# Kernel optimization log

Hardware: AMD Instinct MI355X
Metric: run time of the kernel (lower is better)

## Reference

```python
import jax, jax.numpy as jnp
import numpy as np
from jax import lax


def conv2d(x, w, b=None, stride=1, pad=0, groups=1):
    # x: [N,C,H,W], w: [Cout, Cin/groups, kh, kw]
    out = lax.conv_general_dilated(
        x, w, window_strides=(stride, stride),
        padding=[(pad, pad), (pad, pad)],
        feature_group_count=groups,
        dimension_numbers=('NCHW', 'OIHW', 'NCHW'))
    if b is not None:
        out = out + b[None, :, None, None]
    return out


def deform_conv2d(x, offsets, weight, stride=1, pad=1, dil=1, groups=1):
    # x: [N,C,H,W]; offsets: [N, 2*K, Ho, Wo] with (dy,dx) interleaved per kernel tap
    # weight: [Cout, C/groups, kh, kw]
    N, C, H, W = x.shape
    Cout, Cg, kh, kw = weight.shape
    K = kh * kw
    Ho = (H + 2 * pad - dil * (kh - 1) - 1) // stride + 1
    Wo = (W + 2 * pad - dil * (kw - 1) - 1) // stride + 1

    off = offsets.reshape(N, K, 2, Ho, Wo)
    # base sampling grid: p0 + kernel tap offset
    base_h = (jnp.arange(Ho) * stride - pad).astype(x.dtype)  # [Ho]
    base_w = (jnp.arange(Wo) * stride - pad).astype(x.dtype)  # [Wo]
    ki = jnp.repeat(jnp.arange(kh), kw).astype(x.dtype) * dil  # [K]
    kj = jnp.tile(jnp.arange(kw), kh).astype(x.dtype) * dil    # [K]
    py = base_h[None, None, :, None] + ki[None, :, None, None] + off[:, :, 0]  # [N,K,Ho,Wo]
    px = base_w[None, None, None, :] + kj[None, :, None, None] + off[:, :, 1]  # [N,K,Ho,Wo]

    y0 = jnp.floor(py); x0 = jnp.floor(px)
    wy = py - y0; wx = px - x0  # bilinear weights, [N,K,Ho,Wo]
    y0i = y0.astype(jnp.int32); x0i = x0.astype(jnp.int32)

    xf = x.reshape(N, C, H * W)

    def gather(yi, xi):
        valid = (yi >= 0) & (yi < H) & (xi >= 0) & (xi < W)
        yc = jnp.clip(yi, 0, H - 1)
        xc = jnp.clip(xi, 0, W - 1)
        idx = (yc * W + xc).reshape(N, 1, K * Ho * Wo)
        g = jnp.take_along_axis(xf, idx, axis=2).reshape(N, C, K, Ho, Wo)
        return g * valid.astype(x.dtype)[:, None]  # zero padding outside

    v00 = gather(y0i, x0i)
    v01 = gather(y0i, x0i + 1)
    v10 = gather(y0i + 1, x0i)
    v11 = gather(y0i + 1, x0i + 1)
    wy_ = wy[:, None]; wx_ = wx[:, None]  # [N,1,K,Ho,Wo]
    sampled = (v00 * (1 - wy_) * (1 - wx_) + v01 * (1 - wy_) * wx_
               + v10 * wy_ * (1 - wx_) + v11 * wy_ * wx_)  # [N,C,K,Ho,Wo]

    g = groups
    sampled = sampled.reshape(N, g, Cg, K, Ho, Wo)
    wg = weight.reshape(g, Cout // g, Cg, K)
    out = jnp.einsum('ngckhw,gock->ngohw', sampled, wg)
    return out.reshape(N, Cout, Ho, Wo)


def setup_inputs() -> dict:
    key = jax.random.key(0)
    ks = jax.random.split(key, 6)
    N, C, H, W = 8, 256, 64, 64
    offc = 18  # 2*3*3
    return {
        'x': jax.random.normal(ks[0], (N, C, H, W), jnp.float32),
        'w_adj': jax.random.normal(ks[1], (offc, C, 1, 1), jnp.float32) * 0.05,
        'b_adj': jax.random.normal(ks[2], (offc,), jnp.float32) * 0.05,
        'w_off': jax.random.normal(ks[3], (offc, 1, 3, 3), jnp.float32) * 0.05,
        'b_off': jax.random.normal(ks[4], (offc,), jnp.float32) * 0.05,
        'w_def': jax.random.normal(ks[5], (C, C, 3, 3), jnp.float32) * 0.02,
    }


def reference(x, w_adj, b_adj, w_off, b_off, w_def):
    x_chan = conv2d(x, w_adj, b_adj, stride=1, pad=0)            # 1x1 conv -> 18 ch
    offsets = conv2d(x_chan, w_off, b_off, stride=1, pad=1, groups=18)  # depthwise 3x3
    out = deform_conv2d(x, offsets, w_def, stride=1, pad=1, dil=1, groups=1)
    return out
```

## Files before the change

kernel.cpp:

```cpp
#include <hip/hip_runtime.h>


typedef __attribute__((ext_vector_type(8))) short short8v;
typedef __attribute__((ext_vector_type(4))) float f32x4;

#define NPLANE 4096

__device__ inline unsigned bf16_1(float a) {
    unsigned u = __float_as_uint(a);
    u += 0x7fffu + ((u >> 16) & 1u);
    return u >> 16;
}
__device__ inline unsigned bf16_pair(float a, float b) {
    unsigned ua = __float_as_uint(a); ua += 0x7fffu + ((ua >> 16) & 1u);
    unsigned ub = __float_as_uint(b); ub += 0x7fffu + ((ub >> 16) & 1u);
    return (ua >> 16) | (ub & 0xffff0000u);
}
__device__ inline unsigned cvt_pk(float lo, float hi) {
    unsigned r;
    asm("v_cvt_pk_bf16_f32 %0, %1, %2" : "=v"(r) : "v"(lo), "v"(hi));
    return r;
}
__device__ inline float bl(unsigned u) { return __uint_as_float(u << 16); }
__device__ inline float bh(unsigned u) { return __uint_as_float(u & 0xffff0000u); }

__device__ inline void block_sync_lgkm() {
    asm volatile("s_waitcnt lgkmcnt(0)" ::: "memory");
    __builtin_amdgcn_s_barrier();
    __builtin_amdgcn_sched_barrier(0);
}

__global__ __launch_bounds__(256) void k_prep(const float* __restrict__ x,
                                              const float* __restrict__ w_adj,
                                              const float* __restrict__ b_adj,
                                              const float* __restrict__ w_def,
                                              float* __restrict__ xchan,
                                              ushort* __restrict__ wfrag,
                                              ushort* __restrict__ xT) {
    __shared__ float wsh[256][18];
    __shared__ float part[8][32][19];
    __shared__ unsigned tileU[64][35];
    int b = blockIdx.x;
    int t = threadIdx.x;
    if (b < 1024) {
        for (int i = t; i < 18 * 256; i += 256) {
            int o = i >> 8, c = i & 255;
            wsh[c][o] = w_adj[i];
        }
        __syncthreads();
        int n    = b >> 7;
        int pix0 = (b & 127) << 5;
        int p = t & 31, g = t >> 5;
        const float* xp = x + ((size_t)n << 20) + ((size_t)g << 17) + pix0 + p;
        float acc[18];
#pragma unroll
        for (int o = 0; o < 18; ++o) acc[o] = 0.f;
#pragma unroll 4
        for (int ci = 0; ci < 32; ++ci) {
            float xv = xp[(size_t)ci << 12];
            const float* wr = wsh[(g << 5) + ci];
#pragma unroll
            for (int o = 0; o < 18; ++o) acc[o] = fmaf(xv, wr[o], acc[o]);
        }
#pragma unroll
        for (int o = 0; o < 18; ++o) part[g][p][o] = acc[o];
        __syncthreads();
        for (int i = t; i < 576; i += 256) {
            int o = i >> 5, p2 = i & 31;
            float s = b_adj[o];
#pragma unroll
            for (int g2 = 0; g2 < 8; ++g2) s += part[g2][p2][o];
            xchan[((size_t)n * 18 + o) * NPLANE + pix0 + p2] = s;
        }
    } else if (b < 3328) {
        int idx = (b - 1024) * 256 + t;
        int e     = idx & 7;
        int lane  = (idx >> 3) & 63;
        int ct    = (idx >> 9) & 15;
        int kstep = idx >> 13;
        int cout = ct * 16 + (lane & 15);
        int c    = ((kstep & 7) << 5) + ((lane >> 4) << 3) + e;
        int tap  = kstep >> 3;
        float v = w_def[cout * 2304 + c * 9 + tap];
        wfrag[idx] = (ushort)bf16_1(v);
    } else {
        int bb = b - 3328;
        int n  = bb & 7;
        int cg = (bb >> 3) & 3;
        int pg = bb >> 5;
        int pl = t & 63, c4 = t >> 6;
        const float* src = x + (((size_t)(n * 256 + cg * 64 + c4 * 16)) << 12)
                             + (pg << 6) + pl;
#pragma unroll
        for (int i2 = 0; i2 < 8; ++i2) {
            float f0 = src[(size_t)(2 * i2) << 12];
            float f1 = src[(size_t)(2 * i2 + 1) << 12];
            tileU[pl][c4 * 8 + i2] = bf16_pair(f0, f1);
        }
        __syncthreads();
        int cl2 = t & 31, pr = t >> 5;
        unsigned* dst = (unsigned*)xT;
#pragma unroll
        for (int i = 0; i < 8; ++i) {
            int p2 = pr + (i << 3);
            dst[((size_t)(n << 12) + (pg << 6) + p2) * 128 + (cg << 5) + cl2] =
                tileU[p2][cl2];
        }
    }
}

__global__ __launch_bounds__(256) void k_off(const float* __restrict__ xchan,
                                             const float* __restrict__ w_off,
                                             const float* __restrict__ b_off,
                                             float* __restrict__ off) {
    int idx = blockIdx.x * 256 + threadIdx.x;
    int pix = idx & 4095;
    int w = pix & 63, h = pix >> 6;
    int rest = idx >> 12;
    int oc = rest % 18;
    const float* wp  = w_off + oc * 9;
    const float* src = xchan + (idx & ~4095);
    float acc = b_off[oc];
#pragma unroll
    for (int i = 0; i < 3; ++i) {
        int hh = h - 1 + i;
        if ((unsigned)hh >= 64u) continue;
#pragma unroll
        for (int j = 0; j < 3; ++j) {
            int ww = w - 1 + j;
            if ((unsigned)ww >= 64u) continue;
            acc = fmaf(src[(hh << 6) + ww], wp[i * 3 + j], acc);
        }
    }
    off[idx] = acc;
}

__global__ __launch_bounds__(256) void k_fused(const ushort* __restrict__ xT,
                                               const float* __restrict__ off,
                                               const ushort* __restrict__ wfrag,
                                               float* __restrict__ out) {
    __shared__ __align__(16) ushort colS[2][2][2][64][8];

    int t = threadIdx.x;
    int wv = t >> 6, lane = t & 63;
    int n  = blockIdx.x & 7;
    int tq = blockIdx.x >> 3;

    int ksp  = t >> 7;
    int tile = (t >> 6) & 1;
    int pix  = (t >> 2) & 15;
    int cg   = t & 3;
    int sc   = cg << 3;
    int spix = (tq << 5) + (tile << 4) + pix;
    int sy = spix >> 6, sx = spix & 63;

    const float* offn = off + (((size_t)n * 18) << 12) + spix;
    const ushort* xTn = xT + (((size_t)n) << 12) * 256;

    int wslot = (cg << 4) | ((pix ^ (cg << 1)) & 15);
    ushort* wp0 = &colS[0][ksp][tile][wslot][0];
    ushort* wp1 = &colS[1][ksp][tile][wslot][0];

    float w00, w01, w10, w11;
    unsigned oA, oB, oC, oD;

    auto tap_setup = [&](int tp) {
        float oyv = offn[(size_t)(2 * tp) << 12];
        float oxv = offn[(size_t)(2 * tp + 1) << 12];
        int trow = (tp * 11) >> 5;
        int tcol = tp - trow * 3;
        float py = (float)(sy - 1 + trow) + oyv;
        float px = (float)(sx - 1 + tcol) + oxv;
        float fy = floorf(py), fx = floorf(px);
        int y0 = (int)fy, x0 = (int)fx;
        float wy1 = py - fy, wx1 = px - fx;
        float ay0 = ((unsigned)y0       < 64u) ? 1.f - wy1 : 0.f;
        float ay1 = ((unsigned)(y0 + 1) < 64u) ? wy1 : 0.f;
        float ax0 = ((unsigned)x0       < 64u) ? 1.f - wx1 : 0.f;
        float ax1 = ((unsigned)(x0 + 1) < 64u) ? wx1 : 0.f;
        w00 = ay0 * ax0; w01 = ay0 * ax1; w10 = ay1 * ax0; w11 = ay1 * ax1;
        int yc0 = min(max(y0, 0), 63), yc1 = min(max(y0 + 1, 0), 63);
        int xc0 = min(max(x0, 0), 63), xc1 = min(max(x0 + 1, 0), 63);
        oA = (unsigned)((((yc0 << 6) + xc0) << 8) + sc);
        oB = (unsigned)((((yc0 << 6) + xc1) << 8) + sc);
        oC = (unsigned)((((yc1 << 6) + xc0) << 8) + sc);
        oD = (unsigned)((((yc1 << 6) + xc1) << 8) + sc);
    };

    uint4 gA, gB, gC, gD;
    auto issue = [&](int m) {
        unsigned dd = (unsigned)(((2 * m + ksp) & 7) << 5);
        gA = *(const uint4*)(xTn + oA + dd);
        gB = *(const uint4*)(xTn + oB + dd);
        gC = *(const uint4*)(xTn + oC + dd);
        gD = *(const uint4*)(xTn + oD + dd);
    };
    auto interp_to = [&](ushort* wp) {
        unsigned qa[4] = {gA.x, gA.y, gA.z, gA.w};
        unsigned qb[4] = {gB.x, gB.y, gB.z, gB.w};
        unsigned qc[4] = {gC.x, gC.y, gC.z, gC.w};
        unsigned qd[4] = {gD.x, gD.y, gD.z, gD.w};
        unsigned rr[4];
#pragma unroll
        for (int i = 0; i < 4; ++i) {
            float v0 = w00 * bl(qa[i]) + w01 * bl(qb[i]) +
                       w10 * bl(qc[i]) + w11 * bl(qd[i]);
            float v1 = w00 * bh(qa[i]) + w01 * bh(qb[i]) +
                       w10 * bh(qc[i]) + w11 * bh(qd[i]);
            rr[i] = cvt_pk(v0, v1);
        }
        *(uint4*)wp = make_uint4(rr[0], rr[1], rr[2], rr[3]);
    };

    f32x4 acc[2][4] = {};
    const int ctb = wv << 2;

    short8v bbA[4], bbB[4], bbN[4];
    auto loadW = [&](int ks, short8v* dst) {
        const ushort* wb = wfrag + ((size_t)ks * 16 + ctb) * 512 + (lane << 3);
#pragma unroll
        for (int j = 0; j < 4; ++j)
            dst[j] = *(const short8v*)(wb + (size_t)j * 512);
    };

    const int rslot = ((lane >> 4) << 4) | ((lane & 15) ^ ((lane >> 4) << 1));

    tap_setup(0);
    issue(0);
    interp_to(wp0);
    issue(1);
    loadW(0, bbA);
    block_sync_lgkm();

    for (int bt2 = 0; bt2 < 18; ++bt2) {
#pragma unroll
        for (int ph = 0; ph < 2; ++ph) {
            const int bt = bt2 * 2 + ph;
            const ushort* rb = &colS[ph][0][0][0][0];
            short8v a00 = *(const short8v*)(rb + ((0 * 64 + rslot) << 3));
            short8v a01 = *(const short8v*)(rb + ((1 * 64 + rslot) << 3));
            short8v a10 = *(const short8v*)(rb + ((2 * 64 + rslot) << 3));
            short8v a11 = *(const short8v*)(rb + ((3 * 64 + rslot) << 3));
            loadW(2 * bt + 1, bbB);
            if (bt + 1 < 36) loadW(2 * bt + 2, bbN);
            if (bt + 1 < 36) interp_to(ph ? wp0 : wp1);
            if (bt + 2 < 36) {
                if (((bt + 2) & 3) == 0) tap_setup((bt + 2) >> 2);
                issue(bt + 2);
            }
#pragma unroll
            for (int j = 0; j < 4; ++j) {
                acc[0][j] = __builtin_amdgcn_mfma_f32_16x16x32_bf16(
                    bbA[j], a00, acc[0][j], 0, 0, 0);
                acc[1][j] = __builtin_amdgcn_mfma_f32_16x16x32_bf16(
                    bbA[j], a01, acc[1][j], 0, 0, 0);
            }
#pragma unroll
            for (int j = 0; j < 4; ++j) {
                acc[0][j] = __builtin_amdgcn_mfma_f32_16x16x32_bf16(
                    bbB[j], a10, acc[0][j], 0, 0, 0);
                acc[1][j] = __builtin_amdgcn_mfma_f32_16x16x32_bf16(
                    bbB[j], a11, acc[1][j], 0, 0, 0);
            }
            block_sync_lgkm();
#pragma unroll
            for (int j = 0; j < 4; ++j) bbA[j] = bbN[j];
        }
    }

    int cl = lane & 15;
    int ch = (lane >> 4) << 2;
    float* outn = out + ((size_t)n << 20);
#pragma unroll
    for (int i = 0; i < 2; ++i) {
        int opix = (tq << 5) + (i << 4) + cl;
#pragma unroll
        for (int j = 0; j < 4; ++j) {
            int cout = ((ctb + j) << 4) + ch;
            float* op = outn + ((size_t)cout << 12) + opix;
#pragma unroll
            for (int rr = 0; rr < 4; ++rr) op[(size_t)rr << 12] = acc[i][j][rr];
        }
    }
}

__global__ __launch_bounds__(256) void k_xchan(const float* __restrict__ x,
                                               const float* __restrict__ w_adj,
                                               const float* __restrict__ b_adj,
                                               float* __restrict__ xchan) {
    __shared__ float wsh[256][18];
    __shared__ float part[8][32][19];
    int t = threadIdx.x;
    for (int i = t; i < 18 * 256; i += 256) {
        int o = i >> 8, c = i & 255;
        wsh[c][o] = w_adj[i];
    }
    __syncthreads();
    int n    = blockIdx.x >> 7;
    int pix0 = (blockIdx.x & 127) << 5;
    int p = t & 31, g = t >> 5;
    const float* xp = x + ((size_t)n << 20) + ((size_t)g << 17) + pix0 + p;
    float acc[18];
#pragma unroll
    for (int o = 0; o < 18; ++o) acc[o] = 0.f;
#pragma unroll 4
    for (int ci = 0; ci < 32; ++ci) {
        float xv = xp[(size_t)ci << 12];
        const float* wr = wsh[(g << 5) + ci];
#pragma unroll
        for (int o = 0; o < 18; ++o) acc[o] = fmaf(xv, wr[o], acc[o]);
    }
#pragma unroll
    for (int o = 0; o < 18; ++o) part[g][p][o] = acc[o];
    __syncthreads();
    for (int i = t; i < 576; i += 256) {
        int o = i >> 5, p2 = i & 31;
        float s = b_adj[o];
#pragma unroll
        for (int g2 = 0; g2 < 8; ++g2) s += part[g2][p2][o];
        xchan[((size_t)n * 18 + o) * NPLANE + pix0 + p2] = s;
    }
}

__global__ __launch_bounds__(256) void k_reorder(const float* __restrict__ w_def,
                                                 float* __restrict__ w_t) {
    int idx = blockIdx.x * 256 + threadIdx.x;
    int co = idx & 255;
    int c  = (idx >> 8) & 255;
    int k  = idx >> 16;
    w_t[idx] = w_def[co * 2304 + c * 9 + k];
}

__global__ __launch_bounds__(256) void k_deform(const float* __restrict__ x,
                                                const float* __restrict__ off,
                                                const float* __restrict__ w_t,
                                                float* __restrict__ out) {
    __shared__ float colS[16][64];
    __shared__ float wS[16][128];
    __shared__ int   sy0[64], sx0[64];
    __shared__ float swy[64], swx[64];
    int t   = threadIdx.x;
    int n   = blockIdx.x >> 6;
    int h   = blockIdx.x & 63;
    int co0 = blockIdx.y << 7;
    float acc[4][8];
#pragma unroll
    for (int i = 0; i < 4; ++i)
#pragma unroll
        for (int j = 0; j < 8; ++j) acc[i][j] = 0.f;
    int tp = t & 15, tc = t >> 4;
    int cc_b = t >> 4, p0_b = (t & 15) << 2;
    const float* xn = x + (n << 20);
    for (int k = 0; k < 9; ++k) {
        if (t < 64) {
            const float* offp = off + ((n * 18 + 2 * k) << 12) + (h << 6);
            float oyv = offp[t];
            float oxv = offp[4096 + t];
            float py = (float)(h - 1 + k / 3) + oyv;
            float px = (float)(t - 1 + k % 3) + oxv;
            float fy = floorf(py), fx = floorf(px);
            sy0[t] = (int)fy; sx0[t] = (int)fx;
            swy[t] = py - fy; swx[t] = px - fx;
        }
        for (int c0 = 0; c0 < 256; c0 += 16) {
            __syncthreads();
            const float* base = xn + ((c0 + cc_b) << 12);
#pragma unroll
            for (int u = 0; u < 4; ++u) {
                int p = p0_b + u;
                int y0 = sy0[p], x0 = sx0[p];
                float wy = swy[p], wx = swx[p];
                float v00 = 0.f, v01 = 0.f, v10 = 0.f, v11 = 0.f;
                bool oky0 = (unsigned)y0 < 64u, oky1 = (unsigned)(y0 + 1) < 64u;
                bool okx0 = (unsigned)x0 < 64u, okx1 = (unsigned)(x0 + 1) < 64u;
                int r0 = (y0 << 6) + x0;
                if (oky0 && okx0) v00 = base[r0];
                if (oky0 && okx1) v01 = base[r0 + 1];
                if (oky1 && okx0) v10 = base[r0 + 64];
                if (oky1 && okx1) v11 = base[r0 + 65];
                colS[cc_b][p] = (v00 * (1.f - wx) + v01 * wx) * (1.f - wy) +
                                (v10 * (1.f - wx) + v11 * wx) * wy;
            }
            const float* wt = w_t + (k << 16) + (c0 << 8) + co0;
#pragma unroll
            for (int i = 0; i < 2; ++i) {
                int fi = i * 256 + t;
                int cc = fi >> 5;
                int cf = (fi & 31) << 2;
                *(float4*)&wS[cc][cf] = *(const float4*)&wt[(cc << 8) + cf];
            }
            __syncthreads();
#pragma unroll
            for (int kk = 0; kk < 16; ++kk) {
                float4 cv = *(const float4*)&colS[kk][tp << 2];
                float4 w0 = *(const float4*)&wS[kk][tc << 3];
                float4 w1 = *(const float4*)&wS[kk][(tc << 3) + 4];
                float cva[4] = {cv.x, cv.y, cv.z, cv.w};
                float wa[8]  = {w0.x, w0.y, w0.z, w0.w, w1.x, w1.y, w1.z, w1.w};
#pragma unroll
                for (int i = 0; i < 4; ++i)
#pragma unroll
                    for (int j = 0; j < 8; ++j)
                        acc[i][j] = fmaf(cva[i], wa[j], acc[i][j]);
            }
        }
    }
    int ob = (n << 20) + ((co0 + (tc << 3)) << 12) + (h << 6) + (tp << 2);
#pragma unroll
    for (int j = 0; j < 8; ++j) {
        float4 v = {acc[0][j], acc[1][j], acc[2][j], acc[3][j]};
        *(float4*)&out[ob + (j << 12)] = v;
    }
}

extern "C" void kernel_launch(void* const* d_in, const int* in_sizes, int n_in,
                              void* d_out, int out_size, void* d_ws, size_t ws_size,
                              hipStream_t stream) {
    const float* x     = (const float*)d_in[0];
    const float* w_adj = (const float*)d_in[1];
    const float* b_adj = (const float*)d_in[2];
    const float* w_off = (const float*)d_in[3];
    const float* b_off = (const float*)d_in[4];
    const float* w_def = (const float*)d_in[5];
    float* out = (float*)d_out;

    char* ws = (char*)d_ws;
    float* xchan = (float*)ws;
    float* off   = (float*)(ws + 2359296);

    const size_t NEED = 22675456;
    if (ws_size >= NEED) {
        ushort* wfrag = (ushort*)(ws + 4718592);
        ushort* xT    = (ushort*)(ws + 5898240);
        k_prep<<<5376, 256, 0, stream>>>(x, w_adj, b_adj, w_def,
                                         xchan, wfrag, xT);
        k_off<<<2304, 256, 0, stream>>>(xchan, w_off, b_off, off);
        k_fused<<<1024, 256, 0, stream>>>(xT, off, wfrag, out);
    } else {
        float* w_t = (float*)(ws + 4718592);
        k_xchan<<<1024, 256, 0, stream>>>(x, w_adj, b_adj, xchan);
        k_off<<<2304, 256, 0, stream>>>(xchan, w_off, b_off, off);
        k_reorder<<<2304, 256, 0, stream>>>(w_def, w_t);
        k_deform<<<dim3(512, 2), 256, 0, stream>>>(x, off, w_t, out);
    }
}
```

Baseline: 94.93 us.

## Double pixel tile per block in fused deform conv to reuse weights

Each block of the fused deform-conv GEMM kernel now covers 64 output pixels instead of 32, with all 256 threads sampling distinct pixels rather than splitting the K dimension across two thread halves. Every weight fragment loaded into registers now feeds four MFMA pixel tiles instead of two, so weight traffic per output is halved and the grid shrinks to 512 blocks. The cost is twice as many accumulator registers, twice as many barrier-separated K steps per block, and fewer blocks to spread across the CUs.

```diff
diff --git a/kernel.cpp b/kernel.cpp
--- a/kernel.cpp
+++ b/kernel.cpp
@@ -139,27 +139,26 @@
                                                const float* __restrict__ off,
                                                const ushort* __restrict__ wfrag,
                                                float* __restrict__ out) {
-    __shared__ __align__(16) ushort colS[2][2][2][64][8];
+    __shared__ __align__(16) ushort colS[2][4][64][8];
 
     int t = threadIdx.x;
     int wv = t >> 6, lane = t & 63;
     int n  = blockIdx.x & 7;
     int tq = blockIdx.x >> 3;
 
-    int ksp  = t >> 7;
-    int tile = (t >> 6) & 1;
-    int pix  = (t >> 2) & 15;
-    int cg   = t & 3;
-    int sc   = cg << 3;
-    int spix = (tq << 5) + (tile << 4) + pix;
+    int p6 = t >> 2;
+    int cg = t & 3;
+    int sc = cg << 3;
+    int spix = (tq << 6) + p6;
     int sy = spix >> 6, sx = spix & 63;
 
     const float* offn = off + (((size_t)n * 18) << 12) + spix;
     const ushort* xTn = xT + (((size_t)n) << 12) * 256;
 
-    int wslot = (cg << 4) | ((pix ^ (cg << 1)) & 15);
-    ushort* wp0 = &colS[0][ksp][tile][wslot][0];
-    ushort* wp1 = &colS[1][ksp][tile][wslot][0];
+    int wtile = p6 >> 4;
+    int wslot = (cg << 4) | (((p6 & 15) ^ (cg << 1)) & 15);
+    ushort* wp0 = &colS[0][wtile][wslot][0];
+    ushort* wp1 = &colS[1][wtile][wslot][0];
 
     float w00, w01, w10, w11;
     unsigned oA, oB, oC, oD;
@@ -188,8 +187,8 @@
     };
 
     uint4 gA, gB, gC, gD;
-    auto issue = [&](int m) {
-        unsigned dd = (unsigned)(((2 * m + ksp) & 7) << 5);
+    auto issue = [&](int k) {
+        unsigned dd = (unsigned)((k & 7) << 5);
         gA = *(const uint4*)(xTn + oA + dd);
         gB = *(const uint4*)(xTn + oB + dd);
         gC = *(const uint4*)(xTn + oC + dd);
@@ -212,10 +211,10 @@
         *(uint4*)wp = make_uint4(rr[0], rr[1], rr[2], rr[3]);
     };
 
-    f32x4 acc[2][4] = {};
+    f32x4 acc[4][4] = {};
     const int ctb = wv << 2;
 
-    short8v bbA[4], bbB[4], bbN[4];
+    short8v bbE[4], bbO[4];
     auto loadW = [&](int ks, short8v* dst) {
         const ushort* wb = wfrag + ((size_t)ks * 16 + ctb) * 512 + (lane << 3);
 #pragma unroll
@@ -229,42 +228,37 @@
     issue(0);
     interp_to(wp0);
     issue(1);
-    loadW(0, bbA);
+    loadW(0, bbE);
     block_sync_lgkm();
 
-    for (int bt2 = 0; bt2 < 18; ++bt2) {
+    for (int it = 0; it < 36; ++it) {
 #pragma unroll
         for (int ph = 0; ph < 2; ++ph) {
-            const int bt = bt2 * 2 + ph;
-            const ushort* rb = &colS[ph][0][0][0][0];
-            short8v a00 = *(const short8v*)(rb + ((0 * 64 + rslot) << 3));
-            short8v a01 = *(const short8v*)(rb + ((1 * 64 + rslot) << 3));
-            short8v a10 = *(const short8v*)(rb + ((2 * 64 + rslot) << 3));
-            short8v a11 = *(const short8v*)(rb + ((3 * 64 + rslot) << 3));
-            loadW(2 * bt + 1, bbB);
-            if (bt + 1 < 36) loadW(2 * bt + 2, bbN);
-            if (bt + 1 < 36) interp_to(ph ? wp0 : wp1);
-            if (bt + 2 < 36) {
-                if (((bt + 2) & 3) == 0) tap_setup((bt + 2) >> 2);
-                issue(bt + 2);
+            const int k = it * 2 + ph;
+            const ushort* rb = &colS[ph][0][0][0];
+            short8v a0 = *(const short8v*)(rb + ((0 * 64 + rslot) << 3));
+            short8v a1 = *(const short8v*)(rb + ((1 * 64 + rslot) << 3));
+            short8v a2 = *(const short8v*)(rb + ((2 * 64 + rslot) << 3));
+            short8v a3 = *(const short8v*)(rb + ((3 * 64 + rslot) << 3));
+            if (k + 1 < 72) loadW(k + 1, ph ? bbE : bbO);
+            if (k + 1 < 72) interp_to(ph ? wp0 : wp1);
+            if (k + 2 < 72) {
+                if (((k + 2) & 7) == 0) tap_setup((k + 2) >> 3);
+                issue(k + 2);
             }
+            const short8v* bb = ph ? bbO : bbE;
 #pragma unroll
             for (int j = 0; j < 4; ++j) {
                 acc[0][j] = __builtin_amdgcn_mfma_f32_16x16x32_bf16(
-                    bbA[j], a00, acc[0][j], 0, 0, 0);
+                    bb[j], a0, acc[0][j], 0, 0, 0);
                 acc[1][j] = __builtin_amdgcn_mfma_f32_16x16x32_bf16(
-                    bbA[j], a01, acc[1][j], 0, 0, 0);
-            }
-#pragma unroll
-            for (int j = 0; j < 4; ++j) {
-                acc[0][j] = __builtin_amdgcn_mfma_f32_16x16x32_bf16(
-                    bbB[j], a10, acc[0][j], 0, 0, 0);
-                acc[1][j] = __builtin_amdgcn_mfma_f32_16x16x32_bf16(
-                    bbB[j], a11, acc[1][j], 0, 0, 0);
+                    bb[j], a1, acc[1][j], 0, 0, 0);
+                acc[2][j] = __builtin_amdgcn_mfma_f32_16x16x32_bf16(
+                    bb[j], a2, acc[2][j], 0, 0, 0);
+                acc[3][j] = __builtin_amdgcn_mfma_f32_16x16x32_bf16(
+                    bb[j], a3, acc[3][j], 0, 0, 0);
             }
             block_sync_lgkm();
-#pragma unroll
-            for (int j = 0; j < 4; ++j) bbA[j] = bbN[j];
         }
     }
 
@@ -272,8 +266,8 @@
     int ch = (lane >> 4) << 2;
     float* outn = out + ((size_t)n << 20);
 #pragma unroll
-    for (int i = 0; i < 2; ++i) {
-        int opix = (tq << 5) + (i << 4) + cl;
+    for (int i = 0; i < 4; ++i) {
+        int opix = (tq << 6) + (i << 4) + cl;
 #pragma unroll
         for (int j = 0; j < 4; ++j) {
             int cout = ((ctb + j) << 4) + ch;
@@ -435,7 +429,7 @@
         k_prep<<<5376, 256, 0, stream>>>(x, w_adj, b_adj, w_def,
                                          xchan, wfrag, xT);
         k_off<<<2304, 256, 0, stream>>>(xchan, w_off, b_off, off);
-        k_fused<<<1024, 256, 0, stream>>>(xT, off, wfrag, out);
+        k_fused<<<512, 256, 0, stream>>>(xT, off, wfrag, out);
     } else {
         float* w_t = (float*)(ws + 4718592);
         k_xchan<<<1024, 256, 0, stream>>>(x, w_adj, b_adj, xchan);
```

Result: faster. 84.82 us (-10.7%).

## Enlarge fused deform tile to 64 pixels with 512-thread blocks

Applied to the files above, without the earlier changes.

The fused deformable-conv kernel now processes 64 output pixels per block with 8 waves instead of 32 pixels with 4 waves. Each wave covers 2 output-channel tiles across 4 pixel tiles rather than 4 across 2. This halves the weight fragment loads per wave per step and halves the grid, so each weight fetch feeds more MFMAs. In exchange each block has more threads at the barrier, uses twice the LDS for the sampled columns, and has fewer blocks to spread across CUs.

```diff
diff --git a/kernel.cpp b/kernel.cpp
--- a/kernel.cpp
+++ b/kernel.cpp
@@ -135,31 +135,32 @@
     off[idx] = acc;
 }
 
-__global__ __launch_bounds__(256) void k_fused(const ushort* __restrict__ xT,
+__global__ __launch_bounds__(512) void k_fused(const ushort* __restrict__ xT,
                                                const float* __restrict__ off,
                                                const ushort* __restrict__ wfrag,
                                                float* __restrict__ out) {
-    __shared__ __align__(16) ushort colS[2][2][2][64][8];
+    __shared__ __align__(16) ushort colS[2][2][4][64][8];
 
     int t = threadIdx.x;
     int wv = t >> 6, lane = t & 63;
     int n  = blockIdx.x & 7;
     int tq = blockIdx.x >> 3;
 
-    int ksp  = t >> 7;
-    int tile = (t >> 6) & 1;
-    int pix  = (t >> 2) & 15;
-    int cg   = t & 3;
-    int sc   = cg << 3;
-    int spix = (tq << 5) + (tile << 4) + pix;
+    int ksp = t >> 8;
+    int r_  = t & 255;
+    int p6  = r_ >> 2;
+    int cg  = r_ & 3;
+    int sc  = cg << 3;
+    int spix = (tq << 6) + p6;
     int sy = spix >> 6, sx = spix & 63;
 
     const float* offn = off + (((size_t)n * 18) << 12) + spix;
     const ushort* xTn = xT + (((size_t)n) << 12) * 256;
 
-    int wslot = (cg << 4) | ((pix ^ (cg << 1)) & 15);
-    ushort* wp0 = &colS[0][ksp][tile][wslot][0];
-    ushort* wp1 = &colS[1][ksp][tile][wslot][0];
+    int wtile = p6 >> 4;
+    int wslot = (cg << 4) | (((p6 & 15) ^ (cg << 1)) & 15);
+    ushort* wp0 = &colS[0][ksp][wtile][wslot][0];
+    ushort* wp1 = &colS[1][ksp][wtile][wslot][0];
 
     float w00, w01, w10, w11;
     unsigned oA, oB, oC, oD;
@@ -212,14 +213,14 @@
         *(uint4*)wp = make_uint4(rr[0], rr[1], rr[2], rr[3]);
     };
 
-    f32x4 acc[2][4] = {};
-    const int ctb = wv << 2;
-
-    short8v bbA[4], bbB[4], bbN[4];
+    f32x4 acc[4][2] = {};
+    const int ctb = wv << 1;
+
+    short8v bbA[2], bbB[2], bbN[2];
     auto loadW = [&](int ks, short8v* dst) {
         const ushort* wb = wfrag + ((size_t)ks * 16 + ctb) * 512 + (lane << 3);
 #pragma unroll
-        for (int j = 0; j < 4; ++j)
+        for (int j = 0; j < 2; ++j)
             dst[j] = *(const short8v*)(wb + (size_t)j * 512);
     };
 
@@ -237,10 +238,10 @@
         for (int ph = 0; ph < 2; ++ph) {
             const int bt = bt2 * 2 + ph;
             const ushort* rb = &colS[ph][0][0][0][0];
-            short8v a00 = *(const short8v*)(rb + ((0 * 64 + rslot) << 3));
-            short8v a01 = *(const short8v*)(rb + ((1 * 64 + rslot) << 3));
-            short8v a10 = *(const short8v*)(rb + ((2 * 64 + rslot) << 3));
-            short8v a11 = *(const short8v*)(rb + ((3 * 64 + rslot) << 3));
+            short8v ae0 = *(const short8v*)(rb + ((0 * 64 + rslot) << 3));
+            short8v ae1 = *(const short8v*)(rb + ((1 * 64 + rslot) << 3));
+            short8v ae2 = *(const short8v*)(rb + ((2 * 64 + rslot) << 3));
+            short8v ae3 = *(const short8v*)(rb + ((3 * 64 + rslot) << 3));
             loadW(2 * bt + 1, bbB);
             if (bt + 1 < 36) loadW(2 * bt + 2, bbN);
             if (bt + 1 < 36) interp_to(ph ? wp0 : wp1);
@@ -249,22 +250,34 @@
                 issue(bt + 2);
             }
 #pragma unroll
-            for (int j = 0; j < 4; ++j) {
+            for (int j = 0; j < 2; ++j) {
                 acc[0][j] = __builtin_amdgcn_mfma_f32_16x16x32_bf16(
-                    bbA[j], a00, acc[0][j], 0, 0, 0);
+                    bbA[j], ae0, acc[0][j], 0, 0, 0);
                 acc[1][j] = __builtin_amdgcn_mfma_f32_16x16x32_bf16(
-                    bbA[j], a01, acc[1][j], 0, 0, 0);
-            }
-#pragma unroll
-            for (int j = 0; j < 4; ++j) {
+                    bbA[j], ae1, acc[1][j], 0, 0, 0);
+                acc[2][j] = __builtin_amdgcn_mfma_f32_16x16x32_bf16(
+                    bbA[j], ae2, acc[2][j], 0, 0, 0);
+                acc[3][j] = __builtin_amdgcn_mfma_f32_16x16x32_bf16(
+                    bbA[j], ae3, acc[3][j], 0, 0, 0);
+            }
+            short8v ao0 = *(const short8v*)(rb + (((4 + 0) * 64 + rslot) << 3));
+            short8v ao1 = *(const short8v*)(rb + (((4 + 1) * 64 + rslot) << 3));
+            short8v ao2 = *(const short8v*)(rb + (((4 + 2) * 64 + rslot) << 3));
+            short8v ao3 = *(const short8v*)(rb + (((4 + 3) * 64 + rslot) << 3));
+#pragma unroll
+            for (int j = 0; j < 2; ++j) {
                 acc[0][j] = __builtin_amdgcn_mfma_f32_16x16x32_bf16(
-                    bbB[j], a10, acc[0][j], 0, 0, 0);
+                    bbB[j], ao0, acc[0][j], 0, 0, 0);
                 acc[1][j] = __builtin_amdgcn_mfma_f32_16x16x32_bf16(
-                    bbB[j], a11, acc[1][j], 0, 0, 0);
+                    bbB[j], ao1, acc[1][j], 0, 0, 0);
+                acc[2][j] = __builtin_amdgcn_mfma_f32_16x16x32_bf16(
+                    bbB[j], ao2, acc[2][j], 0, 0, 0);
+                acc[3][j] = __builtin_amdgcn_mfma_f32_16x16x32_bf16(
+                    bbB[j], ao3, acc[3][j], 0, 0, 0);
             }
             block_sync_lgkm();
 #pragma unroll
-            for (int j = 0; j < 4; ++j) bbA[j] = bbN[j];
+            for (int j = 0; j < 2; ++j) bbA[j] = bbN[j];
         }
     }
 
@@ -272,10 +285,10 @@
     int ch = (lane >> 4) << 2;
     float* outn = out + ((size_t)n << 20);
 #pragma unroll
-    for (int i = 0; i < 2; ++i) {
-        int opix = (tq << 5) + (i << 4) + cl;
-#pragma unroll
-        for (int j = 0; j < 4; ++j) {
+    for (int i = 0; i < 4; ++i) {
+        int opix = (tq << 6) + (i << 4) + cl;
+#pragma unroll
+        for (int j = 0; j < 2; ++j) {
             int cout = ((ctb + j) << 4) + ch;
             float* op = outn + ((size_t)cout << 12) + opix;
 #pragma unroll
@@ -435,7 +448,7 @@
         k_prep<<<5376, 256, 0, stream>>>(x, w_adj, b_adj, w_def,
                                          xchan, wfrag, xT);
         k_off<<<2304, 256, 0, stream>>>(xchan, w_off, b_off, off);
-        k_fused<<<1024, 256, 0, stream>>>(xT, off, wfrag, out);
+        k_fused<<<512, 512, 0, stream>>>(xT, off, wfrag, out);
     } else {
         float* w_t = (float*)(ws + 4718592);
         k_xchan<<<1024, 256, 0, stream>>>(x, w_adj, b_adj, xchan);
```

Measured after the change: 83.85 us. 11.7% less time.

## Fuse 1x1 conv with bf16 transpose and enlarge deform GEMM tile to 1024 threads

Applied to the files above, without the earlier changes.

In the prep kernel, the 1x1 offset-channel convolution and the bf16 pixel-major transpose of x now run in the same blocks, so x is read once from global memory instead of twice. The fused deform kernel moves from 256-thread blocks covering 32 pixels to 1024-thread blocks covering 128 pixels, with 16 waves arranged as 4 pixel groups by 4 output-channel groups. Each weight fragment loaded from global memory is therefore reused across more pixels, and the B-fragment double buffering is simplified. The cost is more LDS per block, only 256 blocks for the whole grid, and block-wide barriers across 16 waves, which may hurt occupancy and latency hiding.

```diff
diff --git a/kernel.cpp b/kernel.cpp
--- a/kernel.cpp
+++ b/kernel.cpp
@@ -37,43 +37,56 @@
                                               float* __restrict__ xchan,
                                               ushort* __restrict__ wfrag,
                                               ushort* __restrict__ xT) {
-    __shared__ float wsh[256][18];
-    __shared__ float part[8][32][19];
-    __shared__ unsigned tileU[64][35];
+    __shared__ unsigned tileU[64][133];
+    __shared__ float    ubuf[5120];
     int b = blockIdx.x;
     int t = threadIdx.x;
-    if (b < 1024) {
-        for (int i = t; i < 18 * 256; i += 256) {
+    if (b < 512) {
+        int n  = b & 7;
+        int pg = b >> 3;
+        int pl = t & 63, c4 = t >> 6;
+        for (int i = t; i < 4608; i += 256) {
             int o = i >> 8, c = i & 255;
-            wsh[c][o] = w_adj[i];
+            ubuf[c * 20 + o] = w_adj[i];
         }
         __syncthreads();
-        int n    = b >> 7;
-        int pix0 = (b & 127) << 5;
-        int p = t & 31, g = t >> 5;
-        const float* xp = x + ((size_t)n << 20) + ((size_t)g << 17) + pix0 + p;
-        float acc[18];
-#pragma unroll
-        for (int o = 0; o < 18; ++o) acc[o] = 0.f;
+        const float* xp = x + (((size_t)(n * 256 + c4 * 64)) << 12)
+                            + (pg << 6) + pl;
+        float acc18[18];
+#pragma unroll
+        for (int o = 0; o < 18; ++o) acc18[o] = 0.f;
 #pragma unroll 4
-        for (int ci = 0; ci < 32; ++ci) {
-            float xv = xp[(size_t)ci << 12];
-            const float* wr = wsh[(g << 5) + ci];
-#pragma unroll
-            for (int o = 0; o < 18; ++o) acc[o] = fmaf(xv, wr[o], acc[o]);
-        }
-#pragma unroll
-        for (int o = 0; o < 18; ++o) part[g][p][o] = acc[o];
+        for (int i = 0; i < 32; ++i) {
+            float f0 = xp[(size_t)(2 * i) << 12];
+            float f1 = xp[(size_t)(2 * i + 1) << 12];
+            tileU[pl][c4 * 32 + i] = bf16_pair(f0, f1);
+            const float* wr = ubuf + (c4 * 64 + 2 * i) * 20;
+#pragma unroll
+            for (int o = 0; o < 18; ++o)
+                acc18[o] = fmaf(f0, wr[o], fmaf(f1, wr[20 + o], acc18[o]));
+        }
         __syncthreads();
-        for (int i = t; i < 576; i += 256) {
-            int o = i >> 5, p2 = i & 31;
+#pragma unroll
+        for (int o = 0; o < 18; ++o)
+            ubuf[(c4 * 64 + pl) * 19 + o] = acc18[o];
+        __syncthreads();
+        unsigned* dst = (unsigned*)xT;
+#pragma unroll 8
+        for (int i = 0; i < 32; ++i) {
+            int idx = i * 256 + t;
+            int px = idx >> 7, cu = idx & 127;
+            dst[((size_t)((n << 12) + (pg << 6) + px)) * 128 + cu] =
+                tileU[px][cu];
+        }
+        for (int idx = t; idx < 1152; idx += 256) {
+            int o = idx >> 6, px = idx & 63;
             float s = b_adj[o];
 #pragma unroll
-            for (int g2 = 0; g2 < 8; ++g2) s += part[g2][p2][o];
-            xchan[((size_t)n * 18 + o) * NPLANE + pix0 + p2] = s;
-        }
-    } else if (b < 3328) {
-        int idx = (b - 1024) * 256 + t;
+            for (int g = 0; g < 4; ++g) s += ubuf[(g * 64 + px) * 19 + o];
+            xchan[(((size_t)(n * 18 + o)) << 12) + (pg << 6) + px] = s;
+        }
+    } else {
+        int idx = (b - 512) * 256 + t;
         int e     = idx & 7;
         int lane  = (idx >> 3) & 63;
         int ct    = (idx >> 9) & 15;
@@ -83,29 +96,6 @@
         int tap  = kstep >> 3;
         float v = w_def[cout * 2304 + c * 9 + tap];
         wfrag[idx] = (ushort)bf16_1(v);
-    } else {
-        int bb = b - 3328;
-        int n  = bb & 7;
-        int cg = (bb >> 3) & 3;
-        int pg = bb >> 5;
-        int pl = t & 63, c4 = t >> 6;
-        const float* src = x + (((size_t)(n * 256 + cg * 64 + c4 * 16)) << 12)
-                             + (pg << 6) + pl;
-#pragma unroll
-        for (int i2 = 0; i2 < 8; ++i2) {
-            float f0 = src[(size_t)(2 * i2) << 12];
-            float f1 = src[(size_t)(2 * i2 + 1) << 12];
-            tileU[pl][c4 * 8 + i2] = bf16_pair(f0, f1);
-        }
-        __syncthreads();
-        int cl2 = t & 31, pr = t >> 5;
-        unsigned* dst = (unsigned*)xT;
-#pragma unroll
-        for (int i = 0; i < 8; ++i) {
-            int p2 = pr + (i << 3);
-            dst[((size_t)(n << 12) + (pg << 6) + p2) * 128 + (cg << 5) + cl2] =
-                tileU[p2][cl2];
-        }
     }
 }
 
@@ -135,31 +125,33 @@
     off[idx] = acc;
 }
 
-__global__ __launch_bounds__(256) void k_fused(const ushort* __restrict__ xT,
-                                               const float* __restrict__ off,
-                                               const ushort* __restrict__ wfrag,
-                                               float* __restrict__ out) {
-    __shared__ __align__(16) ushort colS[2][2][2][64][8];
+__global__ __launch_bounds__(1024) void k_fused(const ushort* __restrict__ xT,
+                                                const float* __restrict__ off,
+                                                const ushort* __restrict__ wfrag,
+                                                float* __restrict__ out) {
+    __shared__ __align__(16) ushort colS[2][2][8][64][8];
 
     int t = threadIdx.x;
     int wv = t >> 6, lane = t & 63;
     int n  = blockIdx.x & 7;
     int tq = blockIdx.x >> 3;
-
-    int ksp  = t >> 7;
-    int tile = (t >> 6) & 1;
-    int pix  = (t >> 2) & 15;
-    int cg   = t & 3;
-    int sc   = cg << 3;
-    int spix = (tq << 5) + (tile << 4) + pix;
+    int wp = wv >> 2, wc = wv & 3;
+
+    int ksp = t >> 9;
+    int r_  = t & 511;
+    int p7  = r_ >> 2;
+    int cg  = r_ & 3;
+    int sc  = cg << 3;
+    int spix = (tq << 7) + p7;
     int sy = spix >> 6, sx = spix & 63;
 
     const float* offn = off + (((size_t)n * 18) << 12) + spix;
     const ushort* xTn = xT + (((size_t)n) << 12) * 256;
 
-    int wslot = (cg << 4) | ((pix ^ (cg << 1)) & 15);
-    ushort* wp0 = &colS[0][ksp][tile][wslot][0];
-    ushort* wp1 = &colS[1][ksp][tile][wslot][0];
+    int wtile = p7 >> 4;
+    int wslot = (cg << 4) | (((p7 & 15) ^ (cg << 1)) & 15);
+    ushort* wp0 = &colS[0][ksp][wtile][wslot][0];
+    ushort* wp1 = &colS[1][ksp][wtile][wslot][0];
 
     float w00, w01, w10, w11;
     unsigned oA, oB, oC, oD;
@@ -195,7 +187,7 @@
         gC = *(const uint4*)(xTn + oC + dd);
         gD = *(const uint4*)(xTn + oD + dd);
     };
-    auto interp_to = [&](ushort* wp) {
+    auto interp_to = [&](ushort* wp_) {
         unsigned qa[4] = {gA.x, gA.y, gA.z, gA.w};
         unsigned qb[4] = {gB.x, gB.y, gB.z, gB.w};
         unsigned qc[4] = {gC.x, gC.y, gC.z, gC.w};
@@ -209,15 +201,15 @@
                        w10 * bh(qc[i]) + w11 * bh(qd[i]);
             rr[i] = cvt_pk(v0, v1);
         }
-        *(uint4*)wp = make_uint4(rr[0], rr[1], rr[2], rr[3]);
+        *(uint4*)wp_ = make_uint4(rr[0], rr[1], rr[2], rr[3]);
     };
 
     f32x4 acc[2][4] = {};
-    const int ctb = wv << 2;
-
-    short8v bbA[4], bbB[4], bbN[4];
+
+    short8v bbE[4], bbO[4];
     auto loadW = [&](int ks, short8v* dst) {
-        const ushort* wb = wfrag + ((size_t)ks * 16 + ctb) * 512 + (lane << 3);
+        const ushort* wb = wfrag + ((size_t)ks * 16 + (wc << 2)) * 512
+                                  + (lane << 3);
 #pragma unroll
         for (int j = 0; j < 4; ++j)
             dst[j] = *(const short8v*)(wb + (size_t)j * 512);
@@ -229,7 +221,7 @@
     issue(0);
     interp_to(wp0);
     issue(1);
-    loadW(0, bbA);
+    loadW(0, bbE);
     block_sync_lgkm();
 
     for (int bt2 = 0; bt2 < 18; ++bt2) {
@@ -237,12 +229,9 @@
         for (int ph = 0; ph < 2; ++ph) {
             const int bt = bt2 * 2 + ph;
             const ushort* rb = &colS[ph][0][0][0][0];
-            short8v a00 = *(const short8v*)(rb + ((0 * 64 + rslot) << 3));
-            short8v a01 = *(const short8v*)(rb + ((1 * 64 + rslot) << 3));
-            short8v a10 = *(const short8v*)(rb + ((2 * 64 + rslot) << 3));
-            short8v a11 = *(const short8v*)(rb + ((3 * 64 + rslot) << 3));
-            loadW(2 * bt + 1, bbB);
-            if (bt + 1 < 36) loadW(2 * bt + 2, bbN);
+            short8v ae0 = *(const short8v*)(rb + (((wp * 2 + 0) * 64 + rslot) << 3));
+            short8v ae1 = *(const short8v*)(rb + (((wp * 2 + 1) * 64 + rslot) << 3));
+            loadW(2 * bt + 1, bbO);
             if (bt + 1 < 36) interp_to(ph ? wp0 : wp1);
             if (bt + 2 < 36) {
                 if (((bt + 2) & 3) == 0) tap_setup((bt + 2) >> 2);
@@ -251,20 +240,21 @@
 #pragma unroll
             for (int j = 0; j < 4; ++j) {
                 acc[0][j] = __builtin_amdgcn_mfma_f32_16x16x32_bf16(
-                    bbA[j], a00, acc[0][j], 0, 0, 0);
+                    bbE[j], ae0, acc[0][j], 0, 0, 0);
                 acc[1][j] = __builtin_amdgcn_mfma_f32_16x16x32_bf16(
-                    bbA[j], a01, acc[1][j], 0, 0, 0);
-            }
+                    bbE[j], ae1, acc[1][j], 0, 0, 0);
+            }
+            if (bt + 1 < 36) loadW(2 * bt + 2, bbE);
+            short8v ao0 = *(const short8v*)(rb + (((8 + wp * 2 + 0) * 64 + rslot) << 3));
+            short8v ao1 = *(const short8v*)(rb + (((8 + wp * 2 + 1) * 64 + rslot) << 3));
 #pragma unroll
             for (int j = 0; j < 4; ++j) {
                 acc[0][j] = __builtin_amdgcn_mfma_f32_16x16x32_bf16(
-                    bbB[j], a10, acc[0][j], 0, 0, 0);
+                    bbO[j], ao0, acc[0][j], 0, 0, 0);
                 acc[1][j] = __builtin_amdgcn_mfma_f32_16x16x32_bf16(
-                    bbB[j], a11, acc[1][j], 0, 0, 0);
+                    bbO[j], ao1, acc[1][j], 0, 0, 0);
             }
             block_sync_lgkm();
-#pragma unroll
-            for (int j = 0; j < 4; ++j) bbA[j] = bbN[j];
         }
     }
 
@@ -273,10 +263,10 @@
     float* outn = out + ((size_t)n << 20);
 #pragma unroll
     for (int i = 0; i < 2; ++i) {
-        int opix = (tq << 5) + (i << 4) + cl;
+        int opix = (tq << 7) + (wp << 5) + (i << 4) + cl;
 #pragma unroll
         for (int j = 0; j < 4; ++j) {
-            int cout = ((ctb + j) << 4) + ch;
+            int cout = (((wc << 2) + j) << 4) + ch;
             float* op = outn + ((size_t)cout << 12) + opix;
 #pragma unroll
             for (int rr = 0; rr < 4; ++rr) op[(size_t)rr << 12] = acc[i][j][rr];
@@ -432,10 +422,10 @@
     if (ws_size >= NEED) {
         ushort* wfrag = (ushort*)(ws + 4718592);
         ushort* xT    = (ushort*)(ws + 5898240);
-        k_prep<<<5376, 256, 0, stream>>>(x, w_adj, b_adj, w_def,
+        k_prep<<<2816, 256, 0, stream>>>(x, w_adj, b_adj, w_def,
                                          xchan, wfrag, xT);
         k_off<<<2304, 256, 0, stream>>>(xchan, w_off, b_off, off);
-        k_fused<<<1024, 256, 0, stream>>>(xT, off, wfrag, out);
+        k_fused<<<256, 1024, 0, stream>>>(xT, off, wfrag, out);
     } else {
         float* w_t = (float*)(ws + 4718592);
         k_xchan<<<1024, 256, 0, stream>>>(x, w_adj, b_adj, xchan);
```

Measured after the change: 96.48 us. Within noise of the previous version (+1.6%).
